# Kernel tuning notes

Measured on AMD Instinct MI355X. Metric: run time of the kernel, lower is better.

## Reference

```python
import jax, jax.numpy as jnp
import numpy as np

B, T, C, K = 16, 4096, 64, 1024  # K = codebook rows including pad row 0


def setup_inputs() -> dict:
    key = jax.random.key(0)
    k1, k2, k3 = jax.random.split(key, 3)
    z = jax.random.normal(k1, (B, T, C), dtype=jnp.float32)
    codebook_weight = jax.random.normal(k2, (K, C), dtype=jnp.float32)
    # contiguous valid prefixes of random length (torch loop breaks at first 0)
    lengths = jax.random.randint(k3, (B,), T // 2, T + 1)
    mask = (jnp.arange(T)[None, :] < lengths[:, None]).astype(jnp.float32)[:, :, None]
    return {"z": z, "codebook_weight": codebook_weight, "mask": mask}


def _forward(z, codebook_weight, mask):
    # F.normalize(z, p=2, dim=-1) with eps clamp
    z = z / jnp.clip(jnp.linalg.norm(z, axis=-1, keepdims=True), 1e-12)
    e = jax.lax.stop_gradient(codebook_weight)[1:]  # (K-1, C), detached like torch
    zf = z.reshape(-1, C)                            # (B*T, C)
    # squared euclidean distances: ||z||^2 + ||e||^2 - 2 z e^T
    d = (zf * zf).sum(1, keepdims=True) + (e * e).sum(1)[None, :] - 2.0 * (zf @ e.T)
    idx = jnp.argmin(d, axis=1).reshape(B, T)        # (B, T) codes in [0, K-2]
    # scatter(one-hot) @ e  ==  gather rows of e
    z_q = e[idx] * mask                              # (B, T, C)

    valid_count = mask.sum()
    commitment_loss = (jnp.square(z - jax.lax.stop_gradient(z_q)) * mask).sum() / valid_count

    # straight-through estimator
    z_q = z + z_q - jax.lax.stop_gradient(z)

    m1 = mask[:, 1:, :]
    smoothness_loss = (jnp.square(z_q[:, :-1, :] - z_q[:, 1:, :]) * m1).sum() / m1.sum()

    # --- parallel RLE (replaces the host-side python loop) ---
    # torch loop breaks at first mask==0 -> only contiguous valid prefix matters
    mvalid = jnp.cumprod(mask[..., 0], axis=1) > 0   # (B, T) bool
    change = idx[:, 1:] != idx[:, :-1]
    # position 0 always starts a segment; new segment where code changes inside valid prefix
    is_start = jnp.concatenate(
        [jnp.ones((B, 1), dtype=bool), change & mvalid[:, 1:]], axis=1)  # (B, T)
    # stable argsort puts start positions first, in increasing time order
    order = jnp.argsort(jnp.where(is_start, 0, 1), axis=1)               # (B, T)
    n = is_start.sum(axis=1)                                             # segments per batch
    sel_mask = jnp.arange(T)[None, :] < n[:, None]                        # (B, T)
    sel_pos = jnp.where(sel_mask, order, 0)                               # padded to T
    n_mask = sel_mask.astype(jnp.float32)[..., None]                      # (B, T, 1)
    n_z_q = jnp.take_along_axis(z_q, sel_pos[:, :, None], axis=1) * n_mask
    selected_encodings = jnp.where(
        sel_mask, jnp.take_along_axis(idx, sel_pos, axis=1) + 1, 0)       # (B, T) int
    return smoothness_loss, commitment_loss, z_q, n_z_q, n_mask, selected_encodings


def reference(z, codebook_weight, mask):
    return _forward(z, codebook_weight, mask)
```

## Files before the change

kernel.cpp:

```cpp
#include <hip/hip_runtime.h>
#include <math.h>

typedef __attribute__((ext_vector_type(8))) short short8;
typedef __attribute__((ext_vector_type(4))) float f32x4;

#define B_  16
#define T_  4096
#define C_  64
#define KE_ 1023
#define BT_ (B_ * T_)
#define WINDOW 1e-3f


__device__ __forceinline__ unsigned short f2bf(float x) {
    unsigned int u = __float_as_uint(x);
    unsigned int r = (u + 0x7FFFu + ((u >> 16) & 1u)) >> 16;
    return (unsigned short)r;
}
__device__ __forceinline__ float bf2f(unsigned short h) {
    return __uint_as_float(((unsigned int)h) << 16);
}

__global__ __launch_bounds__(256) void k_prep(const float* __restrict__ cb,
                                              float* __restrict__ ee,
                                              unsigned short* __restrict__ Eh,
                                              unsigned short* __restrict__ El,
                                              int* __restrict__ flagcnt) {
    const int k = blockIdx.x * 256 + threadIdx.x;
    if (k == 0) *flagcnt = 0;
    unsigned int* EhU = (unsigned int*)Eh;
    unsigned int* ElU = (unsigned int*)El;
    if (k < KE_) {
        const float* r = cb + (size_t)(k + 1) * C_;
        float s = 0.f;
        #pragma unroll
        for (int c = 0; c < C_; c += 2) {
            const float x0 = r[c], x1 = r[c + 1];
            s = fmaf(x0, x0, s);
            s = fmaf(x1, x1, s);
            const unsigned short h0 = f2bf(x0), h1 = f2bf(x1);
            const unsigned short l0 = f2bf(x0 - bf2f(h0));
            const unsigned short l1 = f2bf(x1 - bf2f(h1));
            EhU[k * 32 + c / 2] = (unsigned int)h0 | ((unsigned int)h1 << 16);
            ElU[k * 32 + c / 2] = (unsigned int)l0 | ((unsigned int)l1 << 16);
        }
        ee[k] = s;
    } else {
        #pragma unroll
        for (int c = 0; c < 32; ++c) { EhU[k * 32 + c] = 0u; ElU[k * 32 + c] = 0u; }
        ee[k] = INFINITY;
    }
}

__global__ __launch_bounds__(256, 4) void k_assign(
    const float* __restrict__ z, const unsigned short* __restrict__ Eh,
    const unsigned short* __restrict__ El, const float* __restrict__ ee,
    int* __restrict__ kbest, int* __restrict__ flaglist,
    int* __restrict__ flagcnt) {

    __shared__ __align__(16) unsigned short s_eh[128 * 72];
    __shared__ __align__(16) unsigned short s_el[128 * 72];
    __shared__ float s_ee[128];

    const int tid  = threadIdx.x;
    const int wave = tid >> 6;
    const int lane = tid & 63;
    const int col  = lane & 15;
    const int quad = lane >> 4;
    const int Q0   = blockIdx.x * 128 + wave * 32;

    short8 ah[2][2], al[2][2];
    #pragma unroll
    for (int g = 0; g < 2; ++g) {
        const float4* zp = (const float4*)(z + (size_t)(Q0 + g * 16 + col) * C_);
        const float4 f0 = zp[quad * 2];
        const float4 f1 = zp[quad * 2 + 1];
        const float4 f2 = zp[8 + quad * 2];
        const float4 f3 = zp[8 + quad * 2 + 1];
        float xs[16] = {f0.x, f0.y, f0.z, f0.w, f1.x, f1.y, f1.z, f1.w,
                        f2.x, f2.y, f2.z, f2.w, f3.x, f3.y, f3.z, f3.w};
        float ss = 0.f;
        #pragma unroll
        for (int i = 0; i < 16; ++i) ss = fmaf(xs[i], xs[i], ss);
        ss += __shfl_xor(ss, 16);
        ss += __shfl_xor(ss, 32);
        const float inv = 1.f / fmaxf(sqrtf(ss), 1e-12f);
        short8 h0, h1, l0, l1;
        #pragma unroll
        for (int i = 0; i < 8; ++i) {
            const float x = xs[i] * inv;
            const unsigned short hx = f2bf(x);
            h0[i] = (short)hx;
            l0[i] = (short)f2bf(x - bf2f(hx));
            const float y = xs[8 + i] * inv;
            const unsigned short hy = f2bf(y);
            h1[i] = (short)hy;
            l1[i] = (short)f2bf(y - bf2f(hy));
        }
        ah[g][0] = h0; ah[g][1] = h1;
        al[g][0] = l0; al[g][1] = l1;
    }

    float bestv[2][4], secv[2][4];
    int   bkk[2][4];
    #pragma unroll
    for (int g = 0; g < 2; ++g)
        #pragma unroll
        for (int r = 0; r < 4; ++r) {
            bestv[g][r] = INFINITY; secv[g][r] = INFINITY; bkk[g][r] = 0;
        }

    for (int t = 0; t < 8; ++t) {
        __syncthreads();
        #pragma unroll
        for (int j = 0; j < 4; ++j) {
            const int p   = j * 256 + tid;
            const int row = p >> 3;
            const int pc  = p & 7;
            *(uint4*)(&s_eh[row * 72 + pc * 8]) =
                *(const uint4*)(&Eh[(size_t)(t * 128 + row) * 64 + pc * 8]);
            *(uint4*)(&s_el[row * 72 + pc * 8]) =
                *(const uint4*)(&El[(size_t)(t * 128 + row) * 64 + pc * 8]);
        }
        if (tid < 128) s_ee[tid] = ee[t * 128 + tid];
        __syncthreads();

        #pragma unroll 2
        for (int s = 0; s < 8; ++s) {
            const int rbase = (s * 16 + col) * 72 + quad * 8;
            const short8 bh0 = *(const short8*)(&s_eh[rbase]);
            const short8 bh1 = *(const short8*)(&s_eh[rbase + 32]);
            const short8 bl0 = *(const short8*)(&s_el[rbase]);
            const short8 bl1 = *(const short8*)(&s_el[rbase + 32]);
            const float  eev = s_ee[s * 16 + col];

            f32x4 p0 = {0.f, 0.f, 0.f, 0.f}, q0 = {0.f, 0.f, 0.f, 0.f};
            f32x4 p1 = {0.f, 0.f, 0.f, 0.f}, q1 = {0.f, 0.f, 0.f, 0.f};
            p0 = __builtin_amdgcn_mfma_f32_16x16x32_bf16(ah[0][0], bh0, p0, 0, 0, 0);
            p1 = __builtin_amdgcn_mfma_f32_16x16x32_bf16(ah[1][0], bh0, p1, 0, 0, 0);
            q0 = __builtin_amdgcn_mfma_f32_16x16x32_bf16(ah[0][1], bh1, q0, 0, 0, 0);
            q1 = __builtin_amdgcn_mfma_f32_16x16x32_bf16(ah[1][1], bh1, q1, 0, 0, 0);
            p0 = __builtin_amdgcn_mfma_f32_16x16x32_bf16(ah[0][0], bl0, p0, 0, 0, 0);
            p1 = __builtin_amdgcn_mfma_f32_16x16x32_bf16(ah[1][0], bl0, p1, 0, 0, 0);
            q0 = __builtin_amdgcn_mfma_f32_16x16x32_bf16(ah[0][1], bl1, q0, 0, 0, 0);
            q1 = __builtin_amdgcn_mfma_f32_16x16x32_bf16(ah[1][1], bl1, q1, 0, 0, 0);
            p0 = __builtin_amdgcn_mfma_f32_16x16x32_bf16(al[0][0], bh0, p0, 0, 0, 0);
            p1 = __builtin_amdgcn_mfma_f32_16x16x32_bf16(al[1][0], bh0, p1, 0, 0, 0);
            q0 = __builtin_amdgcn_mfma_f32_16x16x32_bf16(al[0][1], bh1, q0, 0, 0, 0);
            q1 = __builtin_amdgcn_mfma_f32_16x16x32_bf16(al[1][1], bh1, q1, 0, 0, 0);

            const int kc = t * 128 + s * 16 + col;
            #pragma unroll
            for (int r = 0; r < 4; ++r) {
                {
                    const float v = fmaf(-2.f, p0[r] + q0[r], eev);
                    const bool lt = v < bestv[0][r];
                    secv[0][r]  = lt ? bestv[0][r] : fminf(secv[0][r], v);
                    bkk[0][r]   = lt ? kc : bkk[0][r];
                    bestv[0][r] = lt ? v : bestv[0][r];
                }
                {
                    const float v = fmaf(-2.f, p1[r] + q1[r], eev);
                    const bool lt = v < bestv[1][r];
                    secv[1][r]  = lt ? bestv[1][r] : fminf(secv[1][r], v);
                    bkk[1][r]   = lt ? kc : bkk[1][r];
                    bestv[1][r] = lt ? v : bestv[1][r];
                }
            }
        }
    }

    #pragma unroll
    for (int g = 0; g < 2; ++g) {
        #pragma unroll
        for (int r = 0; r < 4; ++r) {
            float b  = bestv[g][r], sc = secv[g][r];
            int   k  = bkk[g][r];
            #pragma unroll
            for (int off = 1; off < 16; off <<= 1) {
                const float ob = __shfl_xor(b, off);
                const int   ok = __shfl_xor(k, off);
                const float os = __shfl_xor(sc, off);
                const bool take = (ob < b) || (ob == b && ok < k);
                const float lose = take ? b : ob;
                sc = fminf(fminf(sc, os), lose);
                b  = take ? ob : b;
                k  = take ? ok : k;
            }
            if (col == 0) {
                const int q = Q0 + g * 16 + quad * 4 + r;
                kbest[q] = k;
                if (!(sc - b > WINDOW)) {
                    const int pos = atomicAdd(flagcnt, 1);
                    flaglist[pos] = q;
                }
            }
        }
    }
}

__global__ __launch_bounds__(256) void k_fix(const float* __restrict__ z,
                                             const float* __restrict__ cb,
                                             const float* __restrict__ ee,
                                             const int* __restrict__ flagcnt,
                                             const int* __restrict__ flaglist,
                                             int* __restrict__ kbest) {
    __shared__ float s_z[64];
    __shared__ float s_bv[4];
    __shared__ int   s_bk[4];
    const int tid  = threadIdx.x;
    const int lane = tid & 63;
    const int wave = tid >> 6;
    const int n = *flagcnt;

    for (int i = blockIdx.x; i < n; i += 1024) {
        const int q = flaglist[i];
        __syncthreads();
        if (tid < 16) ((float4*)s_z)[tid] = ((const float4*)(z + (size_t)q * C_))[tid];
        __syncthreads();

        float4 zn[16];
        float ss = 0.f;
        #pragma unroll
        for (int c4 = 0; c4 < 16; ++c4) {
            const float4 v = ((const float4*)s_z)[c4];
            zn[c4] = v;
            ss = fmaf(v.x, v.x, ss); ss = fmaf(v.y, v.y, ss);
            ss = fmaf(v.z, v.z, ss); ss = fmaf(v.w, v.w, ss);
        }
        const float nrm = fmaxf(sqrtf(ss), 1e-12f);
        #pragma unroll
        for (int c4 = 0; c4 < 16; ++c4) {
            zn[c4].x /= nrm; zn[c4].y /= nrm; zn[c4].z /= nrm; zn[c4].w /= nrm;
        }

        const int k0 = tid * 4;
        const float4* e0 = (const float4*)(cb + (size_t)(k0 + 1) * C_);
        const float4* e1 = (const float4*)(cb + (size_t)(k0 + 2) * C_);
        const float4* e2 = (const float4*)(cb + (size_t)(k0 + 3) * C_);
        const float4* e3 = (const float4*)(cb + (size_t)((k0 + 4 <= KE_) ? (k0 + 4) : KE_) * C_);
        float d0 = 0.f, d1 = 0.f, d2 = 0.f, d3 = 0.f;
        #pragma unroll
        for (int c4 = 0; c4 < 16; ++c4) {
            const float4 x = zn[c4];
            const float4 a = e0[c4], b = e1[c4], c = e2[c4], d = e3[c4];
            d0 = fmaf(x.x, a.x, d0); d0 = fmaf(x.y, a.y, d0);
            d0 = fmaf(x.z, a.z, d0); d0 = fmaf(x.w, a.w, d0);
            d1 = fmaf(x.x, b.x, d1); d1 = fmaf(x.y, b.y, d1);
            d1 = fmaf(x.z, b.z, d1); d1 = fmaf(x.w, b.w, d1);
            d2 = fmaf(x.x, c.x, d2); d2 = fmaf(x.y, c.y, d2);
            d2 = fmaf(x.z, c.z, d2); d2 = fmaf(x.w, c.w, d2);
            d3 = fmaf(x.x, d.x, d3); d3 = fmaf(x.y, d.y, d3);
            d3 = fmaf(x.z, d.z, d3); d3 = fmaf(x.w, d.w, d3);
        }
        float bv = INFINITY;
        int   bk = 0;
        float v;
        v = fmaf(-2.f, d0, ee[k0 + 0]); if (v < bv) { bv = v; bk = k0 + 0; }
        v = fmaf(-2.f, d1, ee[k0 + 1]); if (v < bv) { bv = v; bk = k0 + 1; }
        v = fmaf(-2.f, d2, ee[k0 + 2]); if (v < bv) { bv = v; bk = k0 + 2; }
        v = fmaf(-2.f, d3, ee[k0 + 3]); if (v < bv) { bv = v; bk = k0 + 3; }

        #pragma unroll
        for (int off = 32; off > 0; off >>= 1) {
            const float ov = __shfl_down(bv, off);
            const int   ok = __shfl_down(bk, off);
            if (ov < bv || (ov == bv && ok < bk)) { bv = ov; bk = ok; }
        }
        if (lane == 0) { s_bv[wave] = bv; s_bk[wave] = bk; }
        __syncthreads();
        if (tid == 0) {
            float fb = s_bv[0]; int fk = s_bk[0];
            #pragma unroll
            for (int w = 1; w < 4; ++w) {
                if (s_bv[w] < fb || (s_bv[w] == fb && s_bk[w] < fk)) {
                    fb = s_bv[w]; fk = s_bk[w];
                }
            }
            kbest[q] = fk;
        }
    }
}

__global__ __launch_bounds__(256) void k_epi(
    const float* __restrict__ z, const float* __restrict__ cb,
    const float* __restrict__ mask, const int* __restrict__ kbest,
    float* __restrict__ zqo,
    float* __restrict__ commit_part, float* __restrict__ valid_part,
    float* __restrict__ smooth_part) {

    __shared__ float s_red[12];
    const int tid  = threadIdx.x;
    const int lane = tid & 63;
    const int wave = tid >> 6;
    const int q    = blockIdx.x * 256 + tid;

    const int bi = kbest[q];
    const float m     = mask[q];
    const float mnext = (lane != 63) ? mask[q + 1] : 0.f;

    const float4* zp = (const float4*)(z + (size_t)q * C_);
    const float4* er = (const float4*)(cb + (size_t)(bi + 1) * C_);
    float4* zo = (float4*)(zqo + (size_t)q * C_);

    float4 zr[16];
    float ss = 0.f;
    #pragma unroll
    for (int i = 0; i < 16; ++i) {
        float4 v = zp[i];
        zr[i] = v;
        ss = fmaf(v.x, v.x, ss); ss = fmaf(v.y, v.y, ss);
        ss = fmaf(v.z, v.z, ss); ss = fmaf(v.w, v.w, ss);
    }
    const float nrm = fmaxf(sqrtf(ss), 1e-12f);

    float commit = 0.f, sm = 0.f;
    #pragma unroll
    for (int c4 = 0; c4 < 16; ++c4) {
        const float z0 = zr[c4].x / nrm, z1 = zr[c4].y / nrm;
        const float z2 = zr[c4].z / nrm, z3 = zr[c4].w / nrm;
        const float4 e4 = er[c4];
        const float q0 = e4.x * m, q1 = e4.y * m, q2 = e4.z * m, q3 = e4.w * m;
        float4 o;
        o.x = (z0 + q0) - z0;
        o.y = (z1 + q1) - z1;
        o.z = (z2 + q2) - z2;
        o.w = (z3 + q3) - z3;
        zo[c4] = o;
        const float d0 = z0 - q0, d1 = z1 - q1, d2 = z2 - q2, d3 = z3 - q3;
        commit = fmaf(d0, d0, commit); commit = fmaf(d1, d1, commit);
        commit = fmaf(d2, d2, commit); commit = fmaf(d3, d3, commit);
        const float n0 = __shfl_down(o.x, 1);
        const float n1 = __shfl_down(o.y, 1);
        const float n2 = __shfl_down(o.z, 1);
        const float n3 = __shfl_down(o.w, 1);
        const float x0 = o.x - n0, x1 = o.y - n1;
        const float x2 = o.z - n2, x3 = o.w - n3;
        sm = fmaf(x0, x0, sm); sm = fmaf(x1, x1, sm);
        sm = fmaf(x2, x2, sm); sm = fmaf(x3, x3, sm);
    }
    commit *= m;
    sm     *= mnext;
    float vc = m;
    #pragma unroll
    for (int off = 32; off > 0; off >>= 1) {
        commit += __shfl_down(commit, off);
        vc     += __shfl_down(vc, off);
        sm     += __shfl_down(sm, off);
    }
    if (lane == 0) { s_red[wave] = commit; s_red[4 + wave] = vc; s_red[8 + wave] = sm; }
    __syncthreads();
    if (tid == 0) {
        commit_part[blockIdx.x] = s_red[0] + s_red[1] + s_red[2] + s_red[3];
        valid_part[blockIdx.x]  = s_red[4] + s_red[5] + s_red[6] + s_red[7];
        smooth_part[blockIdx.x] = s_red[8] + s_red[9] + s_red[10] + s_red[11];
    }
}

__global__ __launch_bounds__(256) void k_scan(const int* __restrict__ kbest,
                                              const float* __restrict__ mask,
                                              const float* __restrict__ zqo,
                                              int* __restrict__ selpos,
                                              int* __restrict__ nst,
                                              float* __restrict__ smooth_part) {
    __shared__ int cnt[256];
    __shared__ float sred[4];
    const int b = blockIdx.x;
    const int tid = threadIdx.x;
    const int base = b * T_;
    const int t0 = tid * 16;

    int flags = 0, c = 0;
    int prev = (tid == 0) ? -1 : kbest[base + t0 - 1];
    #pragma unroll
    for (int i = 0; i < 16; ++i) {
        const int t = t0 + i;
        const int cur = kbest[base + t];
        const int is = (t == 0) ? 1
                     : ((cur != prev && mask[base + t] > 0.f) ? 1 : 0);
        flags |= is << i;
        c += is;
        prev = cur;
    }
    cnt[tid] = c;
    __syncthreads();
    for (int off = 1; off < 256; off <<= 1) {
        int add = (tid >= off) ? cnt[tid - off] : 0;
        __syncthreads();
        cnt[tid] += add;
        __syncthreads();
    }
    int pos = cnt[tid] - c;
    #pragma unroll
    for (int i = 0; i < 16; ++i) {
        if ((flags >> i) & 1) selpos[base + pos++] = t0 + i;
    }
    if (tid == 255) nst[b] = cnt[255];

    float v = 0.f;
    for (int e = tid; e < 63 * 64; e += 256) {
        const int j = e >> 6, cc = e & 63;
        const int t = j * 64 + 63;
        const int qq = base + t;
        const float d = zqo[(size_t)qq * C_ + cc] - zqo[(size_t)(qq + 1) * C_ + cc];
        v = fmaf(d * mask[qq + 1], d, v);
    }
    #pragma unroll
    for (int off = 32; off > 0; off >>= 1) v += __shfl_down(v, off);
    if ((tid & 63) == 0) sred[tid >> 6] = v;
    __syncthreads();
    if (tid == 0) smooth_part[256 + b] = sred[0] + sred[1] + sred[2] + sred[3];
}

__global__ __launch_bounds__(256) void k_gsel(const float* __restrict__ zqo,
                                              const int* __restrict__ kbest,
                                              const int* __restrict__ selpos,
                                              const int* __restrict__ nst,
                                              float* __restrict__ nzq,
                                              float* __restrict__ nmask,
                                              float* __restrict__ sel) {
    const int gid = blockIdx.x * 256 + threadIdx.x;
    const int b   = gid >> 16;
    const int rem = gid & 65535;
    const int j   = rem >> 4;
    const int c4  = rem & 15;
    const int n   = nst[b];
    float4 v = make_float4(0.f, 0.f, 0.f, 0.f);
    int p = 0;
    if (j < n) {
        p = selpos[b * T_ + j];
        v = ((const float4*)zqo)[((size_t)b * T_ + p) * 16 + c4];
    }
    ((float4*)nzq)[gid] = v;
    if (c4 == 0) {
        float nm = 0.f, s = 0.f;
        if (j < n) { nm = 1.f; s = (float)(kbest[b * T_ + p] + 1); }
        nmask[b * T_ + j] = nm;
        sel[b * T_ + j]   = s;
    }
}

__global__ __launch_bounds__(256) void k_final(const float* __restrict__ commit_part,
                                               const float* __restrict__ valid_part,
                                               const float* __restrict__ smooth_part,
                                               float* __restrict__ out) {
    __shared__ double rc[256];
    __shared__ double rv[256];
    __shared__ double rs[256];
    const int tid = threadIdx.x;
    double sc = (double)commit_part[tid];
    double sv = (double)valid_part[tid];
    double ssm = (double)smooth_part[tid];
    if (tid < 16) ssm += (double)smooth_part[256 + tid];
    rc[tid] = sc; rv[tid] = sv; rs[tid] = ssm;
    __syncthreads();
    for (int off = 128; off > 0; off >>= 1) {
        if (tid < off) {
            rc[tid] += rc[tid + off];
            rv[tid] += rv[tid + off];
            rs[tid] += rs[tid + off];
        }
        __syncthreads();
    }
    if (tid == 0) {
        double valid = rv[0];
        out[0] = (float)(rs[0] / (valid - (double)B_));
        out[1] = (float)(rc[0] / valid);
    }
}

extern "C" void kernel_launch(void* const* d_in, const int* in_sizes, int n_in,
                              void* d_out, int out_size, void* d_ws, size_t ws_size,
                              hipStream_t stream) {
    const float* z    = (const float*)d_in[0];
    const float* cb   = (const float*)d_in[1];
    const float* mask = (const float*)d_in[2];
    float* out = (float*)d_out;
    char* ws = (char*)d_ws;

    int*            flagcnt     = (int*)(ws + 0);
    float*          ee          = (float*)(ws + 64);
    unsigned short* Eh          = (unsigned short*)(ws + 4224);
    unsigned short* El          = (unsigned short*)(ws + 135296);
    int*            kbest       = (int*)(ws + 266368);
    int*            selpos      = (int*)(ws + 528512);
    int*            nst         = (int*)(ws + 790656);
    float*          commit_part = (float*)(ws + 791680);
    float*          valid_part  = (float*)(ws + 792704);
    float*          smooth_part = (float*)(ws + 793728);
    int*            flaglist    = (int*)(ws + 794816);

    float* zqo   = out + 2;
    float* nzq   = zqo + (size_t)BT_ * C_;
    float* nmask = nzq + (size_t)BT_ * C_;
    float* sel   = nmask + BT_;

    k_prep  <<<4,    256, 0, stream>>>(cb, ee, Eh, El, flagcnt);
    k_assign<<<512,  256, 0, stream>>>(z, Eh, El, ee, kbest, flaglist, flagcnt);
    k_fix   <<<1024, 256, 0, stream>>>(z, cb, ee, flagcnt, flaglist, kbest);
    k_epi   <<<256,  256, 0, stream>>>(z, cb, mask, kbest, zqo,
                                       commit_part, valid_part, smooth_part);
    k_scan  <<<B_,   256, 0, stream>>>(kbest, mask, zqo, selpos, nst, smooth_part);
    k_gsel  <<<4096, 256, 0, stream>>>(zqo, kbest, selpos, nst, nzq, nmask, sel);
    k_final <<<1,    256, 0, stream>>>(commit_part, valid_part, smooth_part, out);
}
```

Measured before the change: 157.4 us.

## Fuse fix-up and epilogue into assign kernel, fold final reduction into gather

Ambiguous-argmin fix-ups now run inside each assign block against a block-local flag list, replacing the global atomic list and the separate fix kernel. The epilogue (z_q write, commit and smoothness partials) also runs in the assign block, reusing shared memory for neighbour differences. The final loss reduction moves into block 0 of the gather kernel, taking the launch count from seven to four. The cost is that blocks holding many flagged rows serialise their fix-up loop, and the epilogue work is split across two threads per row.

```diff
diff --git a/kernel.cpp b/kernel.cpp
--- a/kernel.cpp
+++ b/kernel.cpp
@@ -24,10 +24,8 @@
 __global__ __launch_bounds__(256) void k_prep(const float* __restrict__ cb,
                                               float* __restrict__ ee,
                                               unsigned short* __restrict__ Eh,
-                                              unsigned short* __restrict__ El,
-                                              int* __restrict__ flagcnt) {
+                                              unsigned short* __restrict__ El) {
     const int k = blockIdx.x * 256 + threadIdx.x;
-    if (k == 0) *flagcnt = 0;
     unsigned int* EhU = (unsigned int*)Eh;
     unsigned int* ElU = (unsigned int*)El;
     if (k < KE_) {
@@ -53,21 +51,36 @@
 }
 
 __global__ __launch_bounds__(256, 4) void k_assign(
-    const float* __restrict__ z, const unsigned short* __restrict__ Eh,
-    const unsigned short* __restrict__ El, const float* __restrict__ ee,
-    int* __restrict__ kbest, int* __restrict__ flaglist,
-    int* __restrict__ flagcnt) {
-
-    __shared__ __align__(16) unsigned short s_eh[128 * 72];
-    __shared__ __align__(16) unsigned short s_el[128 * 72];
-    __shared__ float s_ee[128];
+    const float* __restrict__ z, const float* __restrict__ cb,
+    const unsigned short* __restrict__ Eh, const unsigned short* __restrict__ El,
+    const float* __restrict__ ee, const float* __restrict__ mask,
+    int* __restrict__ kbest, float* __restrict__ zqo,
+    float* __restrict__ commit_part, float* __restrict__ valid_part,
+    float* __restrict__ smooth_part) {
+
+    __shared__ __align__(16) char smem[37376];
+    unsigned short* s_eh = (unsigned short*)smem;
+    unsigned short* s_el = (unsigned short*)(smem + 18432);
+    float*          s_ee = (float*)(smem + 36864);
+    float*          s_zq = (float*)smem;
+
+    __shared__ int   s_kb[128];
+    __shared__ int   s_flist[128];
+    __shared__ int   s_fcnt;
+    __shared__ float s_z[64];
+    __shared__ float s_bv[4];
+    __shared__ int   s_bk[4];
+    __shared__ float s_red[12];
 
     const int tid  = threadIdx.x;
     const int wave = tid >> 6;
     const int lane = tid & 63;
     const int col  = lane & 15;
     const int quad = lane >> 4;
-    const int Q0   = blockIdx.x * 128 + wave * 32;
+    const int B0   = blockIdx.x * 128;
+    const int Q0   = B0 + wave * 32;
+
+    if (tid == 0) s_fcnt = 0;
 
     short8 ah[2][2], al[2][2];
     #pragma unroll
@@ -188,33 +201,21 @@
                 k  = take ? ok : k;
             }
             if (col == 0) {
-                const int q = Q0 + g * 16 + quad * 4 + r;
-                kbest[q] = k;
+                const int jl = wave * 32 + g * 16 + quad * 4 + r;
+                s_kb[jl] = k;
                 if (!(sc - b > WINDOW)) {
-                    const int pos = atomicAdd(flagcnt, 1);
-                    flaglist[pos] = q;
+                    const int pos = atomicAdd(&s_fcnt, 1);
+                    s_flist[pos] = jl;
                 }
             }
         }
     }
-}
-
-__global__ __launch_bounds__(256) void k_fix(const float* __restrict__ z,
-                                             const float* __restrict__ cb,
-                                             const float* __restrict__ ee,
-                                             const int* __restrict__ flagcnt,
-                                             const int* __restrict__ flaglist,
-                                             int* __restrict__ kbest) {
-    __shared__ float s_z[64];
-    __shared__ float s_bv[4];
-    __shared__ int   s_bk[4];
-    const int tid  = threadIdx.x;
-    const int lane = tid & 63;
-    const int wave = tid >> 6;
-    const int n = *flagcnt;
-
-    for (int i = blockIdx.x; i < n; i += 1024) {
-        const int q = flaglist[i];
+    __syncthreads();
+
+    const int nflag = s_fcnt;
+    for (int i = 0; i < nflag; ++i) {
+        const int jl = s_flist[i];
+        const int q  = B0 + jl;
         __syncthreads();
         if (tid < 16) ((float4*)s_z)[tid] = ((const float4*)(z + (size_t)q * C_))[tid];
         __syncthreads();
@@ -277,71 +278,73 @@
                     fb = s_bv[w]; fk = s_bk[w];
                 }
             }
-            kbest[q] = fk;
-        }
-    }
-}
-
-__global__ __launch_bounds__(256) void k_epi(
-    const float* __restrict__ z, const float* __restrict__ cb,
-    const float* __restrict__ mask, const int* __restrict__ kbest,
-    float* __restrict__ zqo,
-    float* __restrict__ commit_part, float* __restrict__ valid_part,
-    float* __restrict__ smooth_part) {
-
-    __shared__ float s_red[12];
-    const int tid  = threadIdx.x;
-    const int lane = tid & 63;
-    const int wave = tid >> 6;
-    const int q    = blockIdx.x * 256 + tid;
-
-    const int bi = kbest[q];
-    const float m     = mask[q];
-    const float mnext = (lane != 63) ? mask[q + 1] : 0.f;
-
-    const float4* zp = (const float4*)(z + (size_t)q * C_);
-    const float4* er = (const float4*)(cb + (size_t)(bi + 1) * C_);
-    float4* zo = (float4*)(zqo + (size_t)q * C_);
-
-    float4 zr[16];
+            s_kb[jl] = fk;
+        }
+    }
+    __syncthreads();
+
+    if (tid < 128) kbest[B0 + tid] = s_kb[tid];
+
+    const int jq   = tid >> 1;
+    const int half = tid & 1;
+    const int q    = B0 + jq;
+    const int bi   = s_kb[jq];
+    const float m  = mask[q];
+    const float mnext = (jq < 127) ? mask[q + 1] : 0.f;
+
+    const float4* zp = (const float4*)(z + (size_t)q * C_) + half * 8;
+    const float4* er = (const float4*)(cb + (size_t)(bi + 1) * C_) + half * 8;
+    float4* zo = (float4*)(zqo + (size_t)q * C_) + half * 8;
+
+    float4 zr[8];
     float ss = 0.f;
     #pragma unroll
-    for (int i = 0; i < 16; ++i) {
-        float4 v = zp[i];
+    for (int i = 0; i < 8; ++i) {
+        const float4 v = zp[i];
         zr[i] = v;
         ss = fmaf(v.x, v.x, ss); ss = fmaf(v.y, v.y, ss);
         ss = fmaf(v.z, v.z, ss); ss = fmaf(v.w, v.w, ss);
     }
+    ss += __shfl_xor(ss, 1);
     const float nrm = fmaxf(sqrtf(ss), 1e-12f);
 
-    float commit = 0.f, sm = 0.f;
-    #pragma unroll
-    for (int c4 = 0; c4 < 16; ++c4) {
-        const float z0 = zr[c4].x / nrm, z1 = zr[c4].y / nrm;
-        const float z2 = zr[c4].z / nrm, z3 = zr[c4].w / nrm;
-        const float4 e4 = er[c4];
+    float commit = 0.f;
+    float4 ov[8];
+    #pragma unroll
+    for (int i = 0; i < 8; ++i) {
+        const float z0 = zr[i].x / nrm, z1 = zr[i].y / nrm;
+        const float z2 = zr[i].z / nrm, z3 = zr[i].w / nrm;
+        const float4 e4 = er[i];
         const float q0 = e4.x * m, q1 = e4.y * m, q2 = e4.z * m, q3 = e4.w * m;
         float4 o;
         o.x = (z0 + q0) - z0;
         o.y = (z1 + q1) - z1;
         o.z = (z2 + q2) - z2;
         o.w = (z3 + q3) - z3;
-        zo[c4] = o;
+        ov[i] = o;
+        zo[i] = o;
+        ((float4*)s_zq)[jq * 16 + half * 8 + i] = o;
         const float d0 = z0 - q0, d1 = z1 - q1, d2 = z2 - q2, d3 = z3 - q3;
         commit = fmaf(d0, d0, commit); commit = fmaf(d1, d1, commit);
         commit = fmaf(d2, d2, commit); commit = fmaf(d3, d3, commit);
-        const float n0 = __shfl_down(o.x, 1);
-        const float n1 = __shfl_down(o.y, 1);
-        const float n2 = __shfl_down(o.z, 1);
-        const float n3 = __shfl_down(o.w, 1);
-        const float x0 = o.x - n0, x1 = o.y - n1;
-        const float x2 = o.z - n2, x3 = o.w - n3;
-        sm = fmaf(x0, x0, sm); sm = fmaf(x1, x1, sm);
-        sm = fmaf(x2, x2, sm); sm = fmaf(x3, x3, sm);
     }
     commit *= m;
-    sm     *= mnext;
-    float vc = m;
+    __syncthreads();
+
+    float sm = 0.f;
+    if (jq < 127) {
+        #pragma unroll
+        for (int i = 0; i < 8; ++i) {
+            const float4 nb = ((const float4*)s_zq)[(jq + 1) * 16 + half * 8 + i];
+            const float x0 = ov[i].x - nb.x, x1 = ov[i].y - nb.y;
+            const float x2 = ov[i].z - nb.z, x3 = ov[i].w - nb.w;
+            sm = fmaf(x0, x0, sm); sm = fmaf(x1, x1, sm);
+            sm = fmaf(x2, x2, sm); sm = fmaf(x3, x3, sm);
+        }
+        sm *= mnext;
+    }
+    float vc = (half == 0) ? m : 0.f;
+
     #pragma unroll
     for (int off = 32; off > 0; off >>= 1) {
         commit += __shfl_down(commit, off);
@@ -398,9 +401,9 @@
     if (tid == 255) nst[b] = cnt[255];
 
     float v = 0.f;
-    for (int e = tid; e < 63 * 64; e += 256) {
+    for (int e = tid; e < 31 * 64; e += 256) {
         const int j = e >> 6, cc = e & 63;
-        const int t = j * 64 + 63;
+        const int t = j * 128 + 127;
         const int qq = base + t;
         const float d = zqo[(size_t)qq * C_ + cc] - zqo[(size_t)(qq + 1) * C_ + cc];
         v = fmaf(d * mask[qq + 1], d, v);
@@ -409,16 +412,20 @@
     for (int off = 32; off > 0; off >>= 1) v += __shfl_down(v, off);
     if ((tid & 63) == 0) sred[tid >> 6] = v;
     __syncthreads();
-    if (tid == 0) smooth_part[256 + b] = sred[0] + sred[1] + sred[2] + sred[3];
+    if (tid == 0) smooth_part[512 + b] = sred[0] + sred[1] + sred[2] + sred[3];
 }
 
 __global__ __launch_bounds__(256) void k_gsel(const float* __restrict__ zqo,
                                               const int* __restrict__ kbest,
                                               const int* __restrict__ selpos,
                                               const int* __restrict__ nst,
+                                              const float* __restrict__ commit_part,
+                                              const float* __restrict__ valid_part,
+                                              const float* __restrict__ smooth_part,
                                               float* __restrict__ nzq,
                                               float* __restrict__ nmask,
-                                              float* __restrict__ sel) {
+                                              float* __restrict__ sel,
+                                              float* __restrict__ out) {
     const int gid = blockIdx.x * 256 + threadIdx.x;
     const int b   = gid >> 16;
     const int rem = gid & 65535;
@@ -438,34 +445,31 @@
         nmask[b * T_ + j] = nm;
         sel[b * T_ + j]   = s;
     }
-}
-
-__global__ __launch_bounds__(256) void k_final(const float* __restrict__ commit_part,
-                                               const float* __restrict__ valid_part,
-                                               const float* __restrict__ smooth_part,
-                                               float* __restrict__ out) {
-    __shared__ double rc[256];
-    __shared__ double rv[256];
-    __shared__ double rs[256];
-    const int tid = threadIdx.x;
-    double sc = (double)commit_part[tid];
-    double sv = (double)valid_part[tid];
-    double ssm = (double)smooth_part[tid];
-    if (tid < 16) ssm += (double)smooth_part[256 + tid];
-    rc[tid] = sc; rv[tid] = sv; rs[tid] = ssm;
-    __syncthreads();
-    for (int off = 128; off > 0; off >>= 1) {
-        if (tid < off) {
-            rc[tid] += rc[tid + off];
-            rv[tid] += rv[tid + off];
-            rs[tid] += rs[tid + off];
-        }
-        __syncthreads();
-    }
-    if (tid == 0) {
-        double valid = rv[0];
-        out[0] = (float)(rs[0] / (valid - (double)B_));
-        out[1] = (float)(rc[0] / valid);
+
+    if (blockIdx.x == 0) {
+        __shared__ double rc[256];
+        __shared__ double rv[256];
+        __shared__ double rs[256];
+        const int tid = threadIdx.x;
+        double sc = (double)commit_part[tid] + (double)commit_part[tid + 256];
+        double sv = (double)valid_part[tid]  + (double)valid_part[tid + 256];
+        double ssm = (double)smooth_part[tid] + (double)smooth_part[tid + 256];
+        if (tid < 16) ssm += (double)smooth_part[512 + tid];
+        rc[tid] = sc; rv[tid] = sv; rs[tid] = ssm;
+        __syncthreads();
+        for (int off = 128; off > 0; off >>= 1) {
+            if (tid < off) {
+                rc[tid] += rc[tid + off];
+                rv[tid] += rv[tid + off];
+                rs[tid] += rs[tid + off];
+            }
+            __syncthreads();
+        }
+        if (tid == 0) {
+            double valid = rv[0];
+            out[0] = (float)(rs[0] / (valid - (double)B_));
+            out[1] = (float)(rc[0] / valid);
+        }
     }
 }
 
@@ -478,7 +482,6 @@
     float* out = (float*)d_out;
     char* ws = (char*)d_ws;
 
-    int*            flagcnt     = (int*)(ws + 0);
     float*          ee          = (float*)(ws + 64);
     unsigned short* Eh          = (unsigned short*)(ws + 4224);
     unsigned short* El          = (unsigned short*)(ws + 135296);
@@ -486,21 +489,19 @@
     int*            selpos      = (int*)(ws + 528512);
     int*            nst         = (int*)(ws + 790656);
     float*          commit_part = (float*)(ws + 791680);
-    float*          valid_part  = (float*)(ws + 792704);
-    float*          smooth_part = (float*)(ws + 793728);
-    int*            flaglist    = (int*)(ws + 794816);
+    float*          valid_part  = (float*)(ws + 793728);
+    float*          smooth_part = (float*)(ws + 795776);
 
     float* zqo   = out + 2;
     float* nzq   = zqo + (size_t)BT_ * C_;
     float* nmask = nzq + (size_t)BT_ * C_;
     float* sel   = nmask + BT_;
 
-    k_prep  <<<4,    256, 0, stream>>>(cb, ee, Eh, El, flagcnt);
-    k_assign<<<512,  256, 0, stream>>>(z, Eh, El, ee, kbest, flaglist, flagcnt);
-    k_fix   <<<1024, 256, 0, stream>>>(z, cb, ee, flagcnt, flaglist, kbest);
-    k_epi   <<<256,  256, 0, stream>>>(z, cb, mask, kbest, zqo,
+    k_prep  <<<4,    256, 0, stream>>>(cb, ee, Eh, El);
+    k_assign<<<512,  256, 0, stream>>>(z, cb, Eh, El, ee, mask, kbest, zqo,
                                        commit_part, valid_part, smooth_part);
     k_scan  <<<B_,   256, 0, stream>>>(kbest, mask, zqo, selpos, nst, smooth_part);
-    k_gsel  <<<4096, 256, 0, stream>>>(zqo, kbest, selpos, nst, nzq, nmask, sel);
-    k_final <<<1,    256, 0, stream>>>(commit_part, valid_part, smooth_part, out);
-}
+    k_gsel  <<<4096, 256, 0, stream>>>(zqo, kbest, selpos, nst,
+                                       commit_part, valid_part, smooth_part,
+                                       nzq, nmask, sel, out);
+}
```

Result: slower. 191.1 us (+21.4%).
